# Optimization experiments

Measured on AMD Instinct MI355X. Metric: run time of the kernel, lower is better.

## Reference

```python
import jax, jax.numpy as jnp
import numpy as np
from math import factorial, sqrt

L = 8
RCUT = 5.0
PI = 3.14159  # literal used in the torch module's Ylm normalization
N_POINTS = 4194304


def powcmplx(zr, zi, n):
    # Faithful port, including the n>2 recurrence that uses the *updated*
    # real part when forming the imaginary part (as in the source).
    if n == 0:
        return jnp.ones_like(zr), jnp.zeros_like(zr)
    if n == 1:
        return zr, zi
    if n == 2:
        return zr * zr - zi * zi, 2.0 * zr * zi
    r, im = zr, zi
    for _ in range(2, n + 1):
        r = zr * r - zi * im
        im = zr * im + zi * r  # uses updated r, matching the source exactly
    return r, im


def _forward(pos):
    norms = jnp.sqrt(jnp.sum(pos * pos, axis=1))
    valid = norms > 0
    mask = valid.astype(pos.dtype)
    safe = jnp.where(valid, norms, 1.0)
    # cosine_cutoff uses the true pi (acos trick in the source)
    cut = 0.5 * (jnp.cos(norms * (jnp.pi / RCUT)) + 1.0)
    cut = jnp.where(norms > RCUT, 0.0, cut) * mask  # mask replaces boolean row-select
    xp_r = -0.5 * pos[:, 0]
    xp_i = -0.5 * pos[:, 1]
    xm_r = 0.5 * pos[:, 0]
    xm_i = -0.5 * pos[:, 1]
    x0 = pos[:, 2]
    n_out = (L + 1) ** 2
    vals = [jnp.zeros((), pos.dtype)] * n_out
    i = 0
    for l in range(L + 1):
        w_l = cut / safe ** l * sqrt((2 * l + 1) / 4 / PI)  # per-point weight for this l
        for M in range(-l, 1):
            m = abs(M)
            sr = jnp.zeros_like(x0)
            si = jnp.zeros_like(x0)
            for p in range(l + 1):
                q = p - m
                s = l - p - q
                if q >= 0 and s >= 0:
                    z1r, z1i = powcmplx(xp_r, xp_i, p)
                    z2r, z2i = powcmplx(xm_r, xm_i, q)
                    zr = z1r ** 2 - z2i ** 2      # faithful to source (squared terms)
                    zi = z1r * z2i + z1i * z2r
                    c = 1.0 / (factorial(p) * factorial(q) * factorial(s))
                    sr = sr + zr * x0 * c          # source multiplies by x0 (x0**s is unused there)
                    si = si + zi * x0 * c
            f = sqrt(factorial(l + m) * factorial(l - m))
            w = f * w_l
            clm_r = jnp.sum(sr * w)
            clm_i = jnp.sum(si * w)
            if m == 0:
                vals[i] = clm_r
            else:
                fac = sqrt(2.0) * (-1) ** m
                vals[i] = fac * clm_i
                vals[i + 2 * m] = fac * clm_r
            i += 1
        i += l
    return jnp.stack(vals).reshape(-1, 1)


def setup_inputs() -> dict:
    key = jax.random.key(0)
    pos = jax.random.normal(key, (N_POINTS, 3), dtype=jnp.float32) * 2.0
    return {"pos": pos}


def reference(pos):
    return _forward(pos)
```

## Files before the change

kernel.cpp:

```cpp
#include <hip/hip_runtime.h>
#include <math.h>


typedef float f32x2 __attribute__((ext_vector_type(2)));

#define NL 8
#define NBLK 1024
#define NTHR 256

__device__ __forceinline__ f32x2 sp(float v) { return f32x2{v, v}; }

__device__ __forceinline__ f32x2 pkfma(f32x2 a, f32x2 b, f32x2 c) {
    return __builtin_elementwise_fma(a, b, c);
}

__device__ __forceinline__ float waveReduce(float v) {
    v += __shfl_down(v, 32);
    v += __shfl_down(v, 16);
    v += __shfl_down(v, 8);
    v += __shfl_down(v, 4);
    v += __shfl_down(v, 2);
    v += __shfl_down(v, 1);
    return v;
}

__device__ __forceinline__ void point_body(float x, float y, float z,
                                           float* __restrict__ acc0,
                                           f32x2* __restrict__ accp) {
    const float FACT[9] = {1.f, 1.f, 2.f, 6.f, 24.f, 120.f, 720.f, 5040.f, 40320.f};

    const float r2 = x * x + y * y + z * z;
    const bool valid = r2 > 0.0f;
    const float inv0 = __builtin_amdgcn_rsqf(r2);
    const float norm = r2 * inv0;
    float cut = 0.5f * (__cosf(norm * 0.6283185307179586f) + 1.0f);
    cut = (r2 > 25.0f) ? 0.0f : cut;
    cut = valid ? cut : 0.0f;
    const float inv = valid ? inv0 : 1.0f;
    const float x0c = z * cut;

    const f32x2 w  = { -0.5f * x,  0.5f * x };
    const f32x2 wi = { -0.5f * y, -0.5f * y };

    f32x2 zr[9], zi[9];
    zr[0] = sp(1.f); zi[0] = sp(0.f);
    zr[1] = w;       zi[1] = wi;
    zr[2] = w * w - wi * wi;
    zi[2] = (w + w) * wi;
    {
        f32x2 cr = zr[2];
        f32x2 ci = w * wi + wi * cr;
#pragma unroll
        for (int k = 3; k <= NL; ++k) {
            const f32x2 nr = w * cr - wi * ci;
            const f32x2 ni = w * ci + wi * nr;
            cr = nr; ci = ni;
            zr[k] = nr; zi[k] = ni;
        }
    }

    float aa[9], bb[9], cc[9], dd[9], sqa[9];
#pragma unroll
    for (int p = 0; p <= NL; ++p) {
        aa[p] = zr[p].x;
        cc[p] = zr[p].y;
        bb[p] = zi[p].x;
        dd[p] = zi[p].y;
        sqa[p] = aa[p] * aa[p];
    }

    float h[9];
    h[0] = x0c;
#pragma unroll
    for (int l = 1; l <= NL; ++l) h[l] = h[l - 1] * inv;

    {
        float Y0[5];
#pragma unroll
        for (int p = 0; p <= 4; ++p) {
            const float cpq = 1.0f / (FACT[p] * FACT[p]);
            Y0[p] = fmaf(-dd[p], dd[p], sqa[p]) * cpq;
        }
#pragma unroll
        for (int l = 0; l <= NL; ++l) {
            float sr = 0.f;
#pragma unroll
            for (int p = 0; p <= 4; ++p) {
                if (2 * p <= l) {
                    const float is = 1.0f / FACT[l - 2 * p];
                    sr = fmaf(Y0[p], is, sr);
                }
            }
            acc0[l] = fmaf(sr, h[l], acc0[l]);
        }
    }

#pragma unroll
    for (int m = 1; m <= NL; ++m) {
        f32x2 Y[9];
#pragma unroll
        for (int p = 0; p <= NL; ++p) {
            if (p >= m && 2 * p - m <= NL) {
                const int q = p - m;
                const float cpq = 1.0f / (FACT[p] * FACT[q]);
                const float bc = bb[p] * cc[q];
                const f32x2 A = { -dd[q], aa[p] };
                const f32x2 B = {  dd[q], dd[q] };
                const f32x2 C = { sqa[p], bc };
                Y[p] = pkfma(A, B, C) * sp(cpq);
            }
        }
#pragma unroll
        for (int l = m; l <= NL; ++l) {
            f32x2 s = sp(0.f);
#pragma unroll
            for (int p = 0; p <= NL; ++p) {
                if (p >= m && 2 * p - m <= l) {
                    const float is = 1.0f / FACT[l - 2 * p + m];
                    s = pkfma(Y[p], sp(is), s);
                }
            }
            const int ai = l * (l - 1) / 2 + (m - 1);
            accp[ai] = pkfma(s, sp(h[l]), accp[ai]);
        }
    }
}

__global__ __launch_bounds__(256, 1)
void sht_main(const float* __restrict__ pos, float* __restrict__ ws, int n) {
    float acc0[9];
    f32x2 accp[36];
#pragma unroll
    for (int i = 0; i < 9; ++i) acc0[i] = 0.f;
#pragma unroll
    for (int i = 0; i < 36; ++i) accp[i] = sp(0.f);

    const int t = blockIdx.x * NTHR + threadIdx.x;
    const int nthreads = NBLK * NTHR;
    const int nchunks = (n / 8 + nthreads - 1) / nthreads;

    for (int c = 0; c < nchunks; ++c) {
        const int idx = (c * nthreads + t) * 8;
#pragma unroll 1
        for (int k = 0; k < 8; ++k) {
            const int i = idx + k;
            float x, y, z;
            if (i < n) {
                x = pos[3 * i + 0];
                y = pos[3 * i + 1];
                z = pos[3 * i + 2];
            } else {
                x = 0.f; y = 0.f; z = 0.f;
            }
            point_body(x, y, z, acc0, accp);
        }
    }

    __shared__ float red[81][5];
    const int lane = threadIdx.x & 63;
    const int wave = threadIdx.x >> 6;

#pragma unroll
    for (int l = 0; l <= NL; ++l) {
        float vr = waveReduce(acc0[l]);
        if (lane == 0) red[l * l + l][wave] = vr;
    }
#pragma unroll
    for (int m = 1; m <= NL; ++m) {
#pragma unroll
        for (int l = m; l <= NL; ++l) {
            const int ai = l * (l - 1) / 2 + (m - 1);
            float vr = waveReduce(accp[ai].x);
            if (lane == 0) red[l * l + l + m][wave] = vr;
            float vi = waveReduce(accp[ai].y);
            if (lane == 0) red[l * l + l - m][wave] = vi;
        }
    }
    __syncthreads();

    if ((int)threadIdx.x < 81) {
        float s = 0.f;
#pragma unroll
        for (int w = 0; w < 4; ++w) s += red[threadIdx.x][w];
        ws[(size_t)threadIdx.x * NBLK + blockIdx.x] = s;
    }
}

__device__ double dfact(int nn) {
    double r = 1.0;
    for (int i = 2; i <= nn; ++i) r *= (double)i;
    return r;
}

__global__ __launch_bounds__(256)
void sht_finalize(const float* __restrict__ ws, float* __restrict__ out) {
    const int j = blockIdx.x;
    const int t = threadIdx.x;
    float s = 0.f;
#pragma unroll
    for (int k = 0; k < NBLK / 256; ++k)
        s += ws[(size_t)j * NBLK + k * 256 + t];
    s = waveReduce(s);

    __shared__ float red[4];
    const int lane = t & 63, wave = t >> 6;
    if (lane == 0) red[wave] = s;
    __syncthreads();
    if (t == 0) {
        float tot = red[0] + red[1] + red[2] + red[3];
        int l = 0;
        while ((l + 1) * (l + 1) <= j) ++l;
        const int M = j - l * l - l;
        const int m = (M < 0) ? -M : M;
        double sc = sqrt(dfact(l + m) * dfact(l - m)) *
                    sqrt((double)(2 * l + 1) / (4.0 * 3.14159));
        if (m > 0) sc *= sqrt(2.0) * ((m & 1) ? -1.0 : 1.0);
        out[j] = (float)((double)tot * sc);
    }
}

extern "C" void kernel_launch(void* const* d_in, const int* in_sizes, int n_in,
                              void* d_out, int out_size, void* d_ws, size_t ws_size,
                              hipStream_t stream) {
    const float* pos = (const float*)d_in[0];
    const int npts = in_sizes[0] / 3;
    float* ws = (float*)d_ws;
    float* out = (float*)d_out;

    sht_main<<<NBLK, NTHR, 0, stream>>>(pos, ws, npts);
    sht_finalize<<<81, 256, 0, stream>>>(ws, out);
}
```

Baseline: 133.1 us.

## Split harmonic accumulation into low-m and high-m kernels to cut register pressure

The single main kernel is split into two kernels. One accumulates the m=0..2 coefficients and the other the m=3..8 coefficients, each holding fewer accumulators and raising launch bounds to allow 4 blocks per CU. This is meant to lower VGPR pressure and raise occupancy. In exchange, the position data is read twice and the shared preamble (norm, cosine cutoff, complex powers) is computed twice per point.

```diff
diff --git a/kernel.cpp b/kernel.cpp
--- a/kernel.cpp
+++ b/kernel.cpp
@@ -24,9 +24,9 @@
     return v;
 }
 
-__device__ __forceinline__ void point_body(float x, float y, float z,
-                                           float* __restrict__ acc0,
-                                           f32x2* __restrict__ accp) {
+__device__ __forceinline__ void point_body_lo(float x, float y, float z,
+                                              float* __restrict__ acc0,
+                                              f32x2* __restrict__ accp) {
     const float FACT[9] = {1.f, 1.f, 2.f, 6.f, 24.f, 120.f, 720.f, 5040.f, 40320.f};
 
     const float r2 = x * x + y * y + z * z;
@@ -42,6 +42,105 @@
     const f32x2 w  = { -0.5f * x,  0.5f * x };
     const f32x2 wi = { -0.5f * y, -0.5f * y };
 
+    f32x2 zr[6], zi[6];
+    zr[0] = sp(1.f); zi[0] = sp(0.f);
+    zr[1] = w;       zi[1] = wi;
+    zr[2] = w * w - wi * wi;
+    zi[2] = (w + w) * wi;
+    {
+        f32x2 cr = zr[2];
+        f32x2 ci = w * wi + wi * cr;
+#pragma unroll
+        for (int k = 3; k <= 5; ++k) {
+            const f32x2 nr = w * cr - wi * ci;
+            const f32x2 ni = w * ci + wi * nr;
+            cr = nr; ci = ni;
+            zr[k] = nr; zi[k] = ni;
+        }
+    }
+
+    float aa[6], bb[6], cc[6], dd[6], sqa[6];
+#pragma unroll
+    for (int p = 0; p <= 5; ++p) {
+        aa[p] = zr[p].x;  cc[p] = zr[p].y;
+        bb[p] = zi[p].x;  dd[p] = zi[p].y;
+        sqa[p] = aa[p] * aa[p];
+    }
+
+    float h[9];
+    h[0] = x0c;
+#pragma unroll
+    for (int l = 1; l <= NL; ++l) h[l] = h[l - 1] * inv;
+
+    {
+        float Y0[5];
+#pragma unroll
+        for (int p = 0; p <= 4; ++p) {
+            const float cpq = 1.0f / (FACT[p] * FACT[p]);
+            Y0[p] = fmaf(-dd[p], dd[p], sqa[p]) * cpq;
+        }
+#pragma unroll
+        for (int l = 0; l <= NL; ++l) {
+            float sr = 0.f;
+#pragma unroll
+            for (int p = 0; p <= 4; ++p) {
+                if (2 * p <= l) {
+                    const float is = 1.0f / FACT[l - 2 * p];
+                    sr = fmaf(Y0[p], is, sr);
+                }
+            }
+            acc0[l] = fmaf(sr, h[l], acc0[l]);
+        }
+    }
+
+#pragma unroll
+    for (int m = 1; m <= 2; ++m) {
+        f32x2 Y[6];
+#pragma unroll
+        for (int p = 0; p <= 5; ++p) {
+            if (p >= m && 2 * p - m <= NL) {
+                const int q = p - m;
+                const float cpq = 1.0f / (FACT[p] * FACT[q]);
+                const float bc = bb[p] * cc[q];
+                const f32x2 A = { -dd[q], aa[p] };
+                const f32x2 B = {  dd[q], dd[q] };
+                const f32x2 C = { sqa[p], bc };
+                Y[p] = pkfma(A, B, C) * sp(cpq);
+            }
+        }
+#pragma unroll
+        for (int l = m; l <= NL; ++l) {
+            f32x2 s = sp(0.f);
+#pragma unroll
+            for (int p = 0; p <= 5; ++p) {
+                if (p >= m && 2 * p - m <= l) {
+                    const float is = 1.0f / FACT[l - 2 * p + m];
+                    s = pkfma(Y[p], sp(is), s);
+                }
+            }
+            const int ai = (m == 1) ? (l - 1) : (l + 6);
+            accp[ai] = pkfma(s, sp(h[l]), accp[ai]);
+        }
+    }
+}
+
+__device__ __forceinline__ void point_body_hi(float x, float y, float z,
+                                              f32x2* __restrict__ accp) {
+    const float FACT[9] = {1.f, 1.f, 2.f, 6.f, 24.f, 120.f, 720.f, 5040.f, 40320.f};
+
+    const float r2 = x * x + y * y + z * z;
+    const bool valid = r2 > 0.0f;
+    const float inv0 = __builtin_amdgcn_rsqf(r2);
+    const float norm = r2 * inv0;
+    float cut = 0.5f * (__cosf(norm * 0.6283185307179586f) + 1.0f);
+    cut = (r2 > 25.0f) ? 0.0f : cut;
+    cut = valid ? cut : 0.0f;
+    const float inv = valid ? inv0 : 1.0f;
+    const float x0c = z * cut;
+
+    const f32x2 w  = { -0.5f * x,  0.5f * x };
+    const f32x2 wi = { -0.5f * y, -0.5f * y };
+
     f32x2 zr[9], zi[9];
     zr[0] = sp(1.f); zi[0] = sp(0.f);
     zr[1] = w;       zi[1] = wi;
@@ -59,14 +158,16 @@
         }
     }
 
-    float aa[9], bb[9], cc[9], dd[9], sqa[9];
+    float aa[9], bb[9], sqa[9], cc[3], dd[3];
 #pragma unroll
     for (int p = 0; p <= NL; ++p) {
-        aa[p] = zr[p].x;
-        cc[p] = zr[p].y;
-        bb[p] = zi[p].x;
-        dd[p] = zi[p].y;
-        sqa[p] = aa[p] * aa[p];
+        if (p >= 3) {
+            aa[p] = zr[p].x;  bb[p] = zi[p].x;
+            sqa[p] = aa[p] * aa[p];
+        }
+        if (p <= 2) {
+            cc[p] = zr[p].y;  dd[p] = zi[p].y;
+        }
     }
 
     float h[9];
@@ -74,29 +175,9 @@
 #pragma unroll
     for (int l = 1; l <= NL; ++l) h[l] = h[l - 1] * inv;
 
-    {
-        float Y0[5];
-#pragma unroll
-        for (int p = 0; p <= 4; ++p) {
-            const float cpq = 1.0f / (FACT[p] * FACT[p]);
-            Y0[p] = fmaf(-dd[p], dd[p], sqa[p]) * cpq;
-        }
-#pragma unroll
-        for (int l = 0; l <= NL; ++l) {
-            float sr = 0.f;
-#pragma unroll
-            for (int p = 0; p <= 4; ++p) {
-                if (2 * p <= l) {
-                    const float is = 1.0f / FACT[l - 2 * p];
-                    sr = fmaf(Y0[p], is, sr);
-                }
-            }
-            acc0[l] = fmaf(sr, h[l], acc0[l]);
-        }
-    }
-
-#pragma unroll
-    for (int m = 1; m <= NL; ++m) {
+#pragma unroll
+    for (int m = 3; m <= NL; ++m) {
+        const int baseB[9] = {0, 0, 0, 0, 6, 11, 15, 18, 20};
         f32x2 Y[9];
 #pragma unroll
         for (int p = 0; p <= NL; ++p) {
@@ -120,20 +201,20 @@
                     s = pkfma(Y[p], sp(is), s);
                 }
             }
-            const int ai = l * (l - 1) / 2 + (m - 1);
+            const int ai = baseB[m] + (l - m);
             accp[ai] = pkfma(s, sp(h[l]), accp[ai]);
         }
     }
 }
 
-__global__ __launch_bounds__(256, 1)
-void sht_main(const float* __restrict__ pos, float* __restrict__ ws, int n) {
+__global__ __launch_bounds__(256, 4)
+void sht_lo(const float* __restrict__ pos, float* __restrict__ ws, int n) {
     float acc0[9];
-    f32x2 accp[36];
+    f32x2 accp[15];
 #pragma unroll
     for (int i = 0; i < 9; ++i) acc0[i] = 0.f;
 #pragma unroll
-    for (int i = 0; i < 36; ++i) accp[i] = sp(0.f);
+    for (int i = 0; i < 15; ++i) accp[i] = sp(0.f);
 
     const int t = blockIdx.x * NTHR + threadIdx.x;
     const int nthreads = NBLK * NTHR;
@@ -152,7 +233,7 @@
             } else {
                 x = 0.f; y = 0.f; z = 0.f;
             }
-            point_body(x, y, z, acc0, accp);
+            point_body_lo(x, y, z, acc0, accp);
         }
     }
 
@@ -166,10 +247,10 @@
         if (lane == 0) red[l * l + l][wave] = vr;
     }
 #pragma unroll
-    for (int m = 1; m <= NL; ++m) {
+    for (int m = 1; m <= 2; ++m) {
 #pragma unroll
         for (int l = m; l <= NL; ++l) {
-            const int ai = l * (l - 1) / 2 + (m - 1);
+            const int ai = (m == 1) ? (l - 1) : (l + 6);
             float vr = waveReduce(accp[ai].x);
             if (lane == 0) red[l * l + l + m][wave] = vr;
             float vi = waveReduce(accp[ai].y);
@@ -179,10 +260,77 @@
     __syncthreads();
 
     if ((int)threadIdx.x < 81) {
-        float s = 0.f;
-#pragma unroll
-        for (int w = 0; w < 4; ++w) s += red[threadIdx.x][w];
-        ws[(size_t)threadIdx.x * NBLK + blockIdx.x] = s;
+        const int j = threadIdx.x;
+        int l = 0;
+        while ((l + 1) * (l + 1) <= j) ++l;
+        const int M = j - l * l - l;
+        const int am = (M < 0) ? -M : M;
+        if (am <= 2) {
+            float s = 0.f;
+#pragma unroll
+            for (int w2 = 0; w2 < 4; ++w2) s += red[j][w2];
+            ws[(size_t)j * NBLK + blockIdx.x] = s;
+        }
+    }
+}
+
+__global__ __launch_bounds__(256, 4)
+void sht_hi(const float* __restrict__ pos, float* __restrict__ ws, int n) {
+    f32x2 accp[21];
+#pragma unroll
+    for (int i = 0; i < 21; ++i) accp[i] = sp(0.f);
+
+    const int t = blockIdx.x * NTHR + threadIdx.x;
+    const int nthreads = NBLK * NTHR;
+    const int nchunks = (n / 8 + nthreads - 1) / nthreads;
+
+    for (int c = 0; c < nchunks; ++c) {
+        const int idx = (c * nthreads + t) * 8;
+#pragma unroll 1
+        for (int k = 0; k < 8; ++k) {
+            const int i = idx + k;
+            float x, y, z;
+            if (i < n) {
+                x = pos[3 * i + 0];
+                y = pos[3 * i + 1];
+                z = pos[3 * i + 2];
+            } else {
+                x = 0.f; y = 0.f; z = 0.f;
+            }
+            point_body_hi(x, y, z, accp);
+        }
+    }
+
+    __shared__ float red[81][5];
+    const int lane = threadIdx.x & 63;
+    const int wave = threadIdx.x >> 6;
+
+#pragma unroll
+    for (int m = 3; m <= NL; ++m) {
+        const int baseB[9] = {0, 0, 0, 0, 6, 11, 15, 18, 20};
+#pragma unroll
+        for (int l = m; l <= NL; ++l) {
+            const int ai = baseB[m] + (l - m);
+            float vr = waveReduce(accp[ai].x);
+            if (lane == 0) red[l * l + l + m][wave] = vr;
+            float vi = waveReduce(accp[ai].y);
+            if (lane == 0) red[l * l + l - m][wave] = vi;
+        }
+    }
+    __syncthreads();
+
+    if ((int)threadIdx.x < 81) {
+        const int j = threadIdx.x;
+        int l = 0;
+        while ((l + 1) * (l + 1) <= j) ++l;
+        const int M = j - l * l - l;
+        const int am = (M < 0) ? -M : M;
+        if (am >= 3) {
+            float s = 0.f;
+#pragma unroll
+            for (int w2 = 0; w2 < 4; ++w2) s += red[j][w2];
+            ws[(size_t)j * NBLK + blockIdx.x] = s;
+        }
     }
 }
 
@@ -227,6 +375,7 @@
     float* ws = (float*)d_ws;
     float* out = (float*)d_out;
 
-    sht_main<<<NBLK, NTHR, 0, stream>>>(pos, ws, npts);
+    sht_lo<<<NBLK, NTHR, 0, stream>>>(pos, ws, npts);
+    sht_hi<<<NBLK, NTHR, 0, stream>>>(pos, ws, npts);
     sht_finalize<<<81, 256, 0, stream>>>(ws, out);
 }
```

Result: slower. 147.8 us (+11.1%).
